# Kernel optimization log

Hardware: AMD Instinct MI355X
Metric: run time of the kernel (lower is better)

## Reference

```python
import jax, jax.numpy as jnp
import numpy as np

N, E, D, L = 50000, 640000, 128, 3  # nodes, edges, channels, layers
EPS = 1e-5


def setup_inputs() -> dict:
    key = jax.random.key(0)
    ks = jax.random.split(key, 10)
    s = 1.0 / np.sqrt(D)
    inp = {
        "x": jax.random.normal(ks[0], (N, D), dtype=jnp.float32),
        "edge_attr": jax.random.normal(ks[1], (E, D), dtype=jnp.float32),
        "w_self": jax.random.normal(ks[2], (L, D, D), dtype=jnp.float32) * s,
        "b_self": jnp.zeros((L, D), dtype=jnp.float32),
        "w_in": jax.random.normal(ks[3], (L, D, D), dtype=jnp.float32) * s,
        "b_in": jnp.zeros((L, D), dtype=jnp.float32),
        "w_rel": jax.random.normal(ks[4], (L, D, D), dtype=jnp.float32) * s,
        "b_rel": jnp.zeros((L, D), dtype=jnp.float32),
        "bn_gamma": jnp.ones((L - 1, D), dtype=jnp.float32),
        "bn_beta": jnp.zeros((L - 1, D), dtype=jnp.float32),
        "edge_index": jax.random.randint(ks[5], (2, E), 0, N, dtype=jnp.int64),
    }
    return inp


def _batchnorm(h, gamma, beta):
    mu = jnp.mean(h, axis=0)
    var = jnp.mean(jnp.square(h - mu), axis=0)  # biased var (torch BN training)
    return (h - mu) * jax.lax.rsqrt(var + EPS) * gamma + beta


def reference(x, edge_attr, w_self, b_self, w_in, b_in, w_rel, b_rel,
              bn_gamma, bn_beta, edge_index):
    src, dst = edge_index[0], edge_index[1]
    # per-node in-degree for mean aggregation (zero-degree nodes -> 0)
    cnt = jax.ops.segment_sum(jnp.ones((E, 1), x.dtype), dst, num_segments=N)
    denom = jnp.maximum(cnt, 1.0)
    for i in range(L):
        # message: lin_in(x_j * edge_attr)
        msg = jnp.einsum('ed,fd->ef', x[src] * edge_attr, w_in[i]) + b_in[i]
        agg = jax.ops.segment_sum(msg, dst, num_segments=N) / denom  # scatter-mean
        x = agg + jnp.einsum('nd,fd->nf', x, w_self[i]) + b_self[i]
        edge_attr = jnp.einsum('ed,fd->ef', edge_attr, w_rel[i]) + b_rel[i]
        if i < L - 1:
            x = jax.nn.relu(_batchnorm(x, bn_gamma[i], bn_beta[i]))
            # dropout p=0.0 -> identity
    return (x, edge_attr)
```

## Files before the change

### kernel.cpp

```cpp
#include <hip/hip_runtime.h>

#define DD 128

typedef __attribute__((ext_vector_type(8))) short bf16x8;
typedef __attribute__((ext_vector_type(4))) short bf16x4;
typedef __attribute__((ext_vector_type(4))) float f32x4;
typedef unsigned short u16;

__device__ __forceinline__ unsigned short f2bf(float f) {
  union { float f; unsigned u; } v; v.f = f;
  unsigned u = v.u;
  return (unsigned short)((u + 0x7FFFu + ((u >> 16) & 1u)) >> 16);
}
__device__ __forceinline__ float bf2f(unsigned short h) {
  union { unsigned u; float f; } v; v.u = ((unsigned)h) << 16; return v.f;
}
__device__ __forceinline__ bf16x8 pack8(f32x4 a, f32x4 b) {
  bf16x8 r;
  r[0] = (short)f2bf(a.x); r[1] = (short)f2bf(a.y);
  r[2] = (short)f2bf(a.z); r[3] = (short)f2bf(a.w);
  r[4] = (short)f2bf(b.x); r[5] = (short)f2bf(b.y);
  r[6] = (short)f2bf(b.z); r[7] = (short)f2bf(b.w);
  return r;
}

__device__ __forceinline__ bool idx_is64(const int* p) {
  return (p[1] | p[3] | p[5] | p[7]) == 0;
}
__device__ __forceinline__ int ld_idx(const int* p, long long i, bool is64) {
  return is64 ? (int)((const long long*)p)[i] : p[i];
}

__global__ void k_count(const int* __restrict__ idx, int* __restrict__ cnt, int E) {
  int e = blockIdx.x * blockDim.x + threadIdx.x;
  if (e >= E) return;
  bool is64 = idx_is64(idx);
  int d = ld_idx(idx, (long long)E + e, is64);
  atomicAdd(&cnt[d], 1);
}

__global__ __launch_bounds__(1024) void k_scan(const int* __restrict__ cnt,
    int* __restrict__ row_start, int* __restrict__ cursor, int N) {
  __shared__ int part[1024];
  int t = threadIdx.x;
  int chunk = (N + 1023) >> 10;
  int lo = t * chunk, hi = lo + chunk; if (hi > N) hi = N; if (lo > N) lo = N;
  int s = 0;
  for (int i = lo; i < hi; ++i) s += cnt[i];
  part[t] = s;
  __syncthreads();
  for (int off = 1; off < 1024; off <<= 1) {
    int v = (t >= off) ? part[t - off] : 0;
    __syncthreads();
    part[t] += v;
    __syncthreads();
  }
  int run = (t == 0) ? 0 : part[t - 1];
  for (int i = lo; i < hi; ++i) {
    row_start[i] = run; cursor[i] = run; run += cnt[i];
  }
  if (t == 1023) row_start[N] = part[1023];
}

__global__ void k_fill(const int* __restrict__ idx, int* __restrict__ cursor,
                       int* __restrict__ edge_of, int* __restrict__ src_csr, int E) {
  int e = blockIdx.x * blockDim.x + threadIdx.x;
  if (e >= E) return;
  bool is64 = idx_is64(idx);
  int s = ld_idx(idx, e, is64);
  int d = ld_idx(idx, (long long)E + e, is64);
  int pos = atomicAdd(&cursor[d], 1);
  edge_of[pos] = e;
  src_csr[pos] = s;
}

template <int MODE>
__global__ __launch_bounds__(256, 2) void k_relmsg(
    const float* __restrict__ x0, const u16* __restrict__ xbin,
    const float* __restrict__ ea0, const u16* __restrict__ eain,
    u16* __restrict__ eabout, float* __restrict__ eafout,
    u16* __restrict__ m,
    const int* __restrict__ edge_of, const int* __restrict__ src_csr,
    const float* __restrict__ w_rel, const float* __restrict__ b_rel,
    const float* __restrict__ scale, const float* __restrict__ shift,
    int ntE) {
  __shared__ short Wl[16384];
  for (int q = threadIdx.x; q < 4096; q += 256) {
    int off = q * 4;
    int f = off >> 7, d = off & 127;
    f32x4 w = *(const f32x4*)(w_rel + off);
    unsigned byte = ((unsigned)(f * 256 + d * 2)) ^ (unsigned)((f & 7) << 4);
    bf16x4 s4;
    s4[0] = (short)f2bf(w.x); s4[1] = (short)f2bf(w.y);
    s4[2] = (short)f2bf(w.z); s4[3] = (short)f2bf(w.w);
    *(bf16x4*)((char*)Wl + byte) = s4;
  }
  __syncthreads();
  int wave = threadIdx.x >> 6, lane = threadIdx.x & 63;
  int tile = blockIdx.x * 4 + wave;
  if (tile >= ntE) return;
  int r = lane & 15, g = lane >> 4;
  int k0 = tile * 16;
  int pos = r;
  int co = pos * 8;

  bf16x8 a8[4];
  if constexpr (MODE == 0) {
    int er = edge_of[k0 + r];
    const float* rp = ea0 + (size_t)er * DD;
#pragma unroll
    for (int ks = 0; ks < 4; ++ks) {
      const float* p = rp + ks * 32 + g * 8;
      a8[ks] = pack8(*(const f32x4*)p, *(const f32x4*)(p + 4));
    }
  } else {
    const u16* rp = eain + (size_t)(k0 + r) * DD;
#pragma unroll
    for (int ks = 0; ks < 4; ++ks) a8[ks] = *(const bf16x8*)(rp + ks * 32 + g * 8);
  }

  int kk[4], sn[4];
#pragma unroll
  for (int i = 0; i < 4; ++i) { kk[i] = k0 + g + 4 * i; sn[i] = src_csr[kk[i]]; }
  f32x4 xf0[4], xf1[4], ef0[4], ef1[4];
  bf16x8 xb[4], eb[4];
  if constexpr (MODE == 0) {
#pragma unroll
    for (int i = 0; i < 4; ++i) {
      int ei = edge_of[kk[i]];
      const float* xp = x0 + (size_t)sn[i] * DD + co;
      const float* ep = ea0 + (size_t)ei * DD + co;
      xf0[i] = *(const f32x4*)xp; xf1[i] = *(const f32x4*)(xp + 4);
      ef0[i] = *(const f32x4*)ep; ef1[i] = *(const f32x4*)(ep + 4);
    }
  } else {
#pragma unroll
    for (int i = 0; i < 4; ++i) {
      xb[i] = *(const bf16x8*)(xbin + (size_t)sn[i] * DD + co);
      eb[i] = *(const bf16x8*)(eain + (size_t)kk[i] * DD + co);
    }
  }
  float sc[8], sh[8];
  if constexpr (MODE >= 1) {
    f32x4 s0 = *(const f32x4*)(scale + co), s1 = *(const f32x4*)(scale + co + 4);
    f32x4 h0 = *(const f32x4*)(shift + co), h1 = *(const f32x4*)(shift + co + 4);
#pragma unroll
    for (int j = 0; j < 4; ++j) { sc[j] = s0[j]; sc[4 + j] = s1[j]; sh[j] = h0[j]; sh[4 + j] = h1[j]; }
  }

  f32x4 acc[8];
#pragma unroll
  for (int ct = 0; ct < 8; ++ct) acc[ct] = (f32x4){0.f, 0.f, 0.f, 0.f};
#pragma unroll
  for (int ct = 0; ct < 8; ++ct) {
    int f = ct * 16 + r;
    unsigned base = (unsigned)(f * 256);
    unsigned sw = (unsigned)((f & 7) << 4);
#pragma unroll
    for (int ks = 0; ks < 4; ++ks) {
      unsigned byte = (base + (unsigned)(ks * 64 + g * 16)) ^ sw;
      bf16x8 bb = *(const bf16x8*)((const char*)Wl + byte);
      acc[ct] = __builtin_amdgcn_mfma_f32_16x16x32_bf16(a8[ks], bb, acc[ct], 0, 0, 0);
    }
  }

#pragma unroll
  for (int i = 0; i < 4; ++i) {
    bf16x8 mm;
    if constexpr (MODE == 0) {
      f32x4 p0 = xf0[i] * ef0[i], p1 = xf1[i] * ef1[i];
      mm = pack8(p0, p1);
    } else {
#pragma unroll
      for (int j = 0; j < 8; ++j) {
        float xv = fmaxf(bf2f((u16)xb[i][j]) * sc[j] + sh[j], 0.f);
        mm[j] = (short)f2bf(xv * bf2f((u16)eb[i][j]));
      }
    }
    *(bf16x8*)(m + (size_t)kk[i] * DD + co) = mm;
  }

  size_t orow[4];
#pragma unroll
  for (int j = 0; j < 4; ++j) {
    int kr = k0 + g * 4 + j;
    orow[j] = (MODE == 2) ? (size_t)edge_of[kr] : (size_t)kr;
  }
#pragma unroll
  for (int ct = 0; ct < 8; ++ct) {
    int col = ct * 16 + r;
    float bv = b_rel[col];
#pragma unroll
    for (int j = 0; j < 4; ++j) {
      float v = acc[ct][j] + bv;
      if constexpr (MODE == 2) eafout[orow[j] * DD + col] = v;
      else                     eabout[orow[j] * DD + col] = f2bf(v);
    }
  }
}

__global__ __launch_bounds__(256) void k_segsum(const u16* __restrict__ m,
    const int* __restrict__ row_start, u16* __restrict__ agg, int N) {
  int n = blockIdx.x * 4 + (threadIdx.x >> 6);
  if (n >= N) return;
  int lane = threadIdx.x & 63;
  int e4 = lane >> 4, c = lane & 15, co = c * 8;
  int s0 = row_start[n], s1 = row_start[n + 1];
  int len = s1 - s0;
  float acc[8];
#pragma unroll
  for (int j = 0; j < 8; ++j) acc[j] = 0.f;
  for (int kk = e4; kk < len; kk += 4) {
    bf16x8 mv = *(const bf16x8*)(m + (size_t)(s0 + kk) * DD + co);
#pragma unroll
    for (int j = 0; j < 8; ++j) acc[j] += bf2f((u16)mv[j]);
  }
#pragma unroll
  for (int j = 0; j < 8; ++j) {
    float s = acc[j];
    s += __shfl_xor(s, 16);
    s += __shfl_xor(s, 32);
    acc[j] = s;
  }
  if (e4 == 0) {
    float inv = (len > 0) ? 1.0f / (float)len : 0.0f;
    f32x4 lo, hi;
#pragma unroll
    for (int j = 0; j < 4; ++j) { lo[j] = acc[j] * inv; hi[j] = acc[4 + j] * inv; }
    *(bf16x8*)(agg + (size_t)n * DD + co) = pack8(lo, hi);
  }
}

template <typename TX, bool BN, typename TO, bool STATS>
__global__ __launch_bounds__(256, 2) void k_node(const u16* __restrict__ agg,
    const TX* __restrict__ xc, const float* __restrict__ W_in,
    const float* __restrict__ W_self, const float* __restrict__ b_in,
    const float* __restrict__ b_self, const int* __restrict__ row_start,
    const float* __restrict__ scale, const float* __restrict__ shift,
    TO* __restrict__ xn, float* __restrict__ gsum, float* __restrict__ gssq,
    int ntiles) {
  __shared__ short Wl[DD * 256];
  for (int q = threadIdx.x; q < DD * 256 / 4; q += 256) {
    int off = q * 4;
    int f = off >> 8, k = off & 255;
    f32x4 w = (k < 128) ? *(const f32x4*)(W_in + f * 128 + k)
                        : *(const f32x4*)(W_self + f * 128 + (k - 128));
    unsigned byte = ((unsigned)(f * 512 + k * 2)) ^ (unsigned)((f & 7) << 4);
    bf16x4 s4;
    s4[0] = (short)f2bf(w.x); s4[1] = (short)f2bf(w.y);
    s4[2] = (short)f2bf(w.z); s4[3] = (short)f2bf(w.w);
    *(bf16x4*)((char*)Wl + byte) = s4;
  }
  __syncthreads();
  int wave = threadIdx.x >> 6, lane = threadIdx.x & 63;
  int tile = blockIdx.x * 4 + wave;
  if (tile >= ntiles) return;
  int r = lane & 15, g = lane >> 4;
  int arowi = tile * 16 + r;
  const u16* arow = agg + (size_t)arowi * DD;
  const TX* xrow = xc + (size_t)arowi * DD;
  bf16x8 a[8];
#pragma unroll
  for (int ks = 0; ks < 4; ++ks) a[ks] = *(const bf16x8*)(arow + ks * 32 + g * 8);
#pragma unroll
  for (int ks = 0; ks < 4; ++ks) {
    int c0 = ks * 32 + g * 8;
    if constexpr (sizeof(TX) == 2) {
      bf16x8 raw = *(const bf16x8*)(xrow + c0);
      if constexpr (BN) {
        bf16x8 fr;
#pragma unroll
        for (int j = 0; j < 8; ++j) {
          float f = fmaxf(bf2f((u16)raw[j]) * scale[c0 + j] + shift[c0 + j], 0.f);
          fr[j] = (short)f2bf(f);
        }
        a[4 + ks] = fr;
      } else {
        a[4 + ks] = raw;
      }
    } else {
      const float* p = (const float*)xrow + c0;
      a[4 + ks] = pack8(*(const f32x4*)p, *(const f32x4*)(p + 4));
    }
  }
  f32x4 acc[8];
#pragma unroll
  for (int ct = 0; ct < 8; ++ct) acc[ct] = (f32x4){0.f, 0.f, 0.f, 0.f};
#pragma unroll
  for (int ct = 0; ct < 8; ++ct) {
    int f = ct * 16 + r;
    unsigned base = (unsigned)(f * 512);
    unsigned sw = (unsigned)((f & 7) << 4);
#pragma unroll
    for (int ks = 0; ks < 8; ++ks) {
      unsigned byte = (base + (unsigned)(ks * 64 + g * 16)) ^ sw;
      bf16x8 b = *(const bf16x8*)((const char*)Wl + byte);
      acc[ct] = __builtin_amdgcn_mfma_f32_16x16x32_bf16(a[ks], b, acc[ct], 0, 0, 0);
    }
  }
  int nbase = tile * 16;
  float degmask[4];
#pragma unroll
  for (int j = 0; j < 4; ++j) {
    int nn = nbase + g * 4 + j;
    degmask[j] = (row_start[nn + 1] > row_start[nn]) ? 1.0f : 0.0f;
  }
#pragma unroll
  for (int ct = 0; ct < 8; ++ct) {
    int col = ct * 16 + r;
    float bi = b_in[col], bs = b_self[col];
    float s = 0.f, s2 = 0.f;
#pragma unroll
    for (int j = 0; j < 4; ++j) {
      float v = acc[ct][j] + bs + bi * degmask[j];
      if constexpr (sizeof(TO) == 2) xn[(size_t)(nbase + g * 4 + j) * DD + col] = (TO)f2bf(v);
      else                            xn[(size_t)(nbase + g * 4 + j) * DD + col] = (TO)v;
      s += v; s2 += v * v;
    }
    if constexpr (STATS) {
      s += __shfl_xor(s, 16);  s += __shfl_xor(s, 32);
      s2 += __shfl_xor(s2, 16); s2 += __shfl_xor(s2, 32);
      if (g == 0) { atomicAdd(&gsum[col], s); atomicAdd(&gssq[col], s2); }
    }
  }
}

__global__ void k_bnfin(float* __restrict__ gsum, float* __restrict__ gssq,
    const float* __restrict__ gamma, const float* __restrict__ beta,
    float* __restrict__ scale, float* __restrict__ shift, int N) {
  int d = threadIdx.x;
  float mu = gsum[d] / (float)N;
  float var = gssq[d] / (float)N - mu * mu;
  float rs = rsqrtf(var + 1e-5f);
  float sc = rs * gamma[d];
  scale[d] = sc;
  shift[d] = beta[d] - mu * sc;
  gsum[d] = 0.f;
  gssq[d] = 0.f;
}

static inline size_t alignup(size_t v, size_t a) { return (v + a - 1) & ~(a - 1); }

extern "C" void kernel_launch(void* const* d_in, const int* in_sizes, int n_in,
                              void* d_out, int out_size, void* d_ws, size_t ws_size,
                              hipStream_t stream) {
  const float* x0     = (const float*)d_in[0];
  const float* ea0    = (const float*)d_in[1];
  const float* w_self = (const float*)d_in[2];
  const float* b_self = (const float*)d_in[3];
  const float* w_in   = (const float*)d_in[4];
  const float* b_in   = (const float*)d_in[5];
  const float* w_rel  = (const float*)d_in[6];
  const float* b_rel  = (const float*)d_in[7];
  const float* gamma  = (const float*)d_in[8];
  const float* beta   = (const float*)d_in[9];
  const int*   idx    = (const int*)d_in[10];

  const int N = in_sizes[0] / DD;
  const int E = in_sizes[1] / DD;

  char* w = (char*)d_ws;
  size_t off = 0;
  int* cnt       = (int*)(w + off); off = alignup(off + (size_t)N * 4, 256);
  int* row_start = (int*)(w + off); off = alignup(off + (size_t)(N + 1) * 4, 256);
  int* cursor    = (int*)(w + off); off = alignup(off + (size_t)N * 4, 256);
  int* edge_of   = (int*)(w + off); off = alignup(off + (size_t)E * 4, 256);
  int* src_csr   = (int*)(w + off); off = alignup(off + (size_t)E * 4, 256);
  float* gstats  = (float*)(w + off); off = alignup(off + 256 * 4, 256);
  float* scale   = (float*)(w + off); off = alignup(off + 128 * 4, 256);
  float* shift   = (float*)(w + off); off = alignup(off + 128 * 4, 256);
  u16* agg       = (u16*)(w + off); off = alignup(off + (size_t)N * DD * 2, 256);
  u16* xbA       = (u16*)(w + off); off = alignup(off + (size_t)N * DD * 2, 256);
  u16* xbB       = (u16*)(w + off); off = alignup(off + (size_t)N * DD * 2, 256);
  u16* eaA       = (u16*)(w + off); off = alignup(off + (size_t)E * DD * 2, 256);
  u16* eaB       = (u16*)(w + off); off = alignup(off + (size_t)E * DD * 2, 256);
  u16* mbuf      = (u16*)(w + off); off = alignup(off + (size_t)E * DD * 2, 256);
  float* gsum = gstats, *gssq = gstats + 128;
  (void)ws_size; (void)n_in; (void)out_size;

  float* out_x  = (float*)d_out;
  float* out_ea = out_x + (size_t)N * DD;

  (void)hipMemsetAsync(cnt, 0, (size_t)N * 4, stream);
  int ethreads = 256, eblocks = (E + ethreads - 1) / ethreads;
  k_count<<<eblocks, ethreads, 0, stream>>>(idx, cnt, E);
  k_scan<<<1, 1024, 0, stream>>>(cnt, row_start, cursor, N);
  k_fill<<<eblocks, ethreads, 0, stream>>>(idx, cursor, edge_of, src_csr, E);
  (void)hipMemsetAsync(gstats, 0, 256 * 4, stream);

  const int ntN = N / 16;
  const int ntE = E / 16;
  const int rmBlocks = (ntE + 3) / 4;
  const int segBlocks = (N + 3) / 4;
  const int nodeBlocks = (ntN + 3) / 4;

  k_relmsg<0><<<rmBlocks, 256, 0, stream>>>(x0, nullptr, ea0, nullptr,
      eaA, nullptr, mbuf, edge_of, src_csr, w_rel, b_rel, scale, shift, ntE);
  k_segsum<<<segBlocks, 256, 0, stream>>>(mbuf, row_start, agg, N);
  k_node<float, false, u16, true><<<nodeBlocks, 256, 0, stream>>>(agg, x0,
      w_in, w_self, b_in, b_self, row_start, scale, shift, xbA, gsum, gssq, ntN);
  k_bnfin<<<1, 128, 0, stream>>>(gsum, gssq, gamma, beta, scale, shift, N);

  k_relmsg<1><<<rmBlocks, 256, 0, stream>>>(nullptr, xbA, nullptr, eaA,
      eaB, nullptr, mbuf, edge_of, src_csr,
      w_rel + DD * DD, b_rel + DD, scale, shift, ntE);
  k_segsum<<<segBlocks, 256, 0, stream>>>(mbuf, row_start, agg, N);
  k_node<u16, true, u16, true><<<nodeBlocks, 256, 0, stream>>>(agg, xbA,
      w_in + DD * DD, w_self + DD * DD, b_in + DD, b_self + DD,
      row_start, scale, shift, xbB, gsum, gssq, ntN);
  k_bnfin<<<1, 128, 0, stream>>>(gsum, gssq, gamma + DD, beta + DD, scale, shift, N);

  k_relmsg<2><<<rmBlocks, 256, 0, stream>>>(nullptr, xbB, nullptr, eaB,
      nullptr, out_ea, mbuf, edge_of, src_csr,
      w_rel + 2 * DD * DD, b_rel + 2 * DD, scale, shift, ntE);
  k_segsum<<<segBlocks, 256, 0, stream>>>(mbuf, row_start, agg, N);
  k_node<u16, true, float, false><<<nodeBlocks, 256, 0, stream>>>(agg, xbB,
      w_in + 2 * DD * DD, w_self + 2 * DD * DD, b_in + 2 * DD, b_self + 2 * DD,
      row_start, scale, shift, out_x, gsum, gssq, ntN);
}
```

Measured before the change: 1.136 ms.

## Process edges in source-sorted order and scatter messages to dst-CSR positions

Edges are now ordered by source node for the message/relation kernel, so x[src] gathers hit the same rows consecutively and gain cache locality. A permutation array maps each source-sorted edge to its destination-CSR slot, and messages are written there so segment-sum still reads contiguous rows. This adds a second count, scan and cursor pass in the preprocessing, one more index load per edge, and scattered writes of the message rows. The edge_attr working layout also changes from dst-sorted to src-sorted order across layers.

```diff
diff --git a/kernel.cpp b/kernel.cpp
--- a/kernel.cpp
+++ b/kernel.cpp
@@ -31,16 +31,19 @@
   return is64 ? (int)((const long long*)p)[i] : p[i];
 }
 
-__global__ void k_count(const int* __restrict__ idx, int* __restrict__ cnt, int E) {
+__global__ void k_count(const int* __restrict__ idx, int* __restrict__ cntD,
+                        int* __restrict__ cntS, int E) {
   int e = blockIdx.x * blockDim.x + threadIdx.x;
   if (e >= E) return;
   bool is64 = idx_is64(idx);
+  int s = ld_idx(idx, e, is64);
   int d = ld_idx(idx, (long long)E + e, is64);
-  atomicAdd(&cnt[d], 1);
+  atomicAdd(&cntD[d], 1);
+  atomicAdd(&cntS[s], 1);
 }
 
 __global__ __launch_bounds__(1024) void k_scan(const int* __restrict__ cnt,
-    int* __restrict__ row_start, int* __restrict__ cursor, int N) {
+    int* __restrict__ base, int* __restrict__ cursor, int N) {
   __shared__ int part[1024];
   int t = threadIdx.x;
   int chunk = (N + 1023) >> 10;
@@ -57,30 +60,34 @@
   }
   int run = (t == 0) ? 0 : part[t - 1];
   for (int i = lo; i < hi; ++i) {
-    row_start[i] = run; cursor[i] = run; run += cnt[i];
-  }
-  if (t == 1023) row_start[N] = part[1023];
-}
-
-__global__ void k_fill(const int* __restrict__ idx, int* __restrict__ cursor,
-                       int* __restrict__ edge_of, int* __restrict__ src_csr, int E) {
+    base[i] = run; cursor[i] = run; run += cnt[i];
+  }
+  if (t == 1023) base[N] = part[1023];
+}
+
+__global__ void k_fill(const int* __restrict__ idx, int* __restrict__ cursorD,
+                       int* __restrict__ cursorS, int* __restrict__ ss_edge,
+                       int* __restrict__ ss_src, int* __restrict__ pos_csr, int E) {
   int e = blockIdx.x * blockDim.x + threadIdx.x;
   if (e >= E) return;
   bool is64 = idx_is64(idx);
   int s = ld_idx(idx, e, is64);
   int d = ld_idx(idx, (long long)E + e, is64);
-  int pos = atomicAdd(&cursor[d], 1);
-  edge_of[pos] = e;
-  src_csr[pos] = s;
+  int pd = atomicAdd(&cursorD[d], 1);
+  int ps = atomicAdd(&cursorS[s], 1);
+  ss_edge[ps] = e;
+  ss_src[ps] = s;
+  pos_csr[ps] = pd;
 }
 
 template <int MODE>
-__global__ __launch_bounds__(256, 2) void k_relmsg(
+__global__ __launch_bounds__(256, 2) void k_gm(
     const float* __restrict__ x0, const u16* __restrict__ xbin,
     const float* __restrict__ ea0, const u16* __restrict__ eain,
     u16* __restrict__ eabout, float* __restrict__ eafout,
     u16* __restrict__ m,
-    const int* __restrict__ edge_of, const int* __restrict__ src_csr,
+    const int* __restrict__ ss_edge, const int* __restrict__ ss_src,
+    const int* __restrict__ pos_csr,
     const float* __restrict__ w_rel, const float* __restrict__ b_rel,
     const float* __restrict__ scale, const float* __restrict__ shift,
     int ntE) {
@@ -101,12 +108,11 @@
   if (tile >= ntE) return;
   int r = lane & 15, g = lane >> 4;
   int k0 = tile * 16;
-  int pos = r;
-  int co = pos * 8;
+  int co = r * 8;
 
   bf16x8 a8[4];
   if constexpr (MODE == 0) {
-    int er = edge_of[k0 + r];
+    int er = ss_edge[k0 + r];
     const float* rp = ea0 + (size_t)er * DD;
 #pragma unroll
     for (int ks = 0; ks < 4; ++ks) {
@@ -119,15 +125,19 @@
     for (int ks = 0; ks < 4; ++ks) a8[ks] = *(const bf16x8*)(rp + ks * 32 + g * 8);
   }
 
-  int kk[4], sn[4];
-#pragma unroll
-  for (int i = 0; i < 4; ++i) { kk[i] = k0 + g + 4 * i; sn[i] = src_csr[kk[i]]; }
+  int kk[4], sn[4], pc[4];
+#pragma unroll
+  for (int i = 0; i < 4; ++i) {
+    kk[i] = k0 + g + 4 * i;
+    sn[i] = ss_src[kk[i]];
+    pc[i] = pos_csr[kk[i]];
+  }
   f32x4 xf0[4], xf1[4], ef0[4], ef1[4];
   bf16x8 xb[4], eb[4];
   if constexpr (MODE == 0) {
 #pragma unroll
     for (int i = 0; i < 4; ++i) {
-      int ei = edge_of[kk[i]];
+      int ei = ss_edge[kk[i]];
       const float* xp = x0 + (size_t)sn[i] * DD + co;
       const float* ep = ea0 + (size_t)ei * DD + co;
       xf0[i] = *(const f32x4*)xp; xf1[i] = *(const f32x4*)(xp + 4);
@@ -177,14 +187,14 @@
         mm[j] = (short)f2bf(xv * bf2f((u16)eb[i][j]));
       }
     }
-    *(bf16x8*)(m + (size_t)kk[i] * DD + co) = mm;
+    *(bf16x8*)(m + (size_t)pc[i] * DD + co) = mm;
   }
 
   size_t orow[4];
 #pragma unroll
   for (int j = 0; j < 4; ++j) {
     int kr = k0 + g * 4 + j;
-    orow[j] = (MODE == 2) ? (size_t)edge_of[kr] : (size_t)kr;
+    orow[j] = (MODE == 2) ? (size_t)ss_edge[kr] : (size_t)kr;
   }
 #pragma unroll
   for (int ct = 0; ct < 8; ++ct) {
@@ -361,11 +371,15 @@
 
   char* w = (char*)d_ws;
   size_t off = 0;
-  int* cnt       = (int*)(w + off); off = alignup(off + (size_t)N * 4, 256);
+  int* cntD      = (int*)(w + off); off = alignup(off + (size_t)N * 4, 256);
+  int* cntS      = (int*)(w + off); off = alignup(off + (size_t)N * 4, 256);
   int* row_start = (int*)(w + off); off = alignup(off + (size_t)(N + 1) * 4, 256);
-  int* cursor    = (int*)(w + off); off = alignup(off + (size_t)N * 4, 256);
-  int* edge_of   = (int*)(w + off); off = alignup(off + (size_t)E * 4, 256);
-  int* src_csr   = (int*)(w + off); off = alignup(off + (size_t)E * 4, 256);
+  int* col_start = (int*)(w + off); off = alignup(off + (size_t)(N + 1) * 4, 256);
+  int* cursorD   = (int*)(w + off); off = alignup(off + (size_t)N * 4, 256);
+  int* cursorS   = (int*)(w + off); off = alignup(off + (size_t)N * 4, 256);
+  int* ss_edge   = (int*)(w + off); off = alignup(off + (size_t)E * 4, 256);
+  int* ss_src    = (int*)(w + off); off = alignup(off + (size_t)E * 4, 256);
+  int* pos_csr   = (int*)(w + off); off = alignup(off + (size_t)E * 4, 256);
   float* gstats  = (float*)(w + off); off = alignup(off + 256 * 4, 256);
   float* scale   = (float*)(w + off); off = alignup(off + 128 * 4, 256);
   float* shift   = (float*)(w + off); off = alignup(off + 128 * 4, 256);
@@ -381,28 +395,32 @@
   float* out_x  = (float*)d_out;
   float* out_ea = out_x + (size_t)N * DD;
 
-  (void)hipMemsetAsync(cnt, 0, (size_t)N * 4, stream);
+  (void)hipMemsetAsync(cntD, 0, (size_t)N * 4, stream);
+  (void)hipMemsetAsync(cntS, 0, (size_t)N * 4, stream);
   int ethreads = 256, eblocks = (E + ethreads - 1) / ethreads;
-  k_count<<<eblocks, ethreads, 0, stream>>>(idx, cnt, E);
-  k_scan<<<1, 1024, 0, stream>>>(cnt, row_start, cursor, N);
-  k_fill<<<eblocks, ethreads, 0, stream>>>(idx, cursor, edge_of, src_csr, E);
+  k_count<<<eblocks, ethreads, 0, stream>>>(idx, cntD, cntS, E);
+  k_scan<<<1, 1024, 0, stream>>>(cntD, row_start, cursorD, N);
+  k_scan<<<1, 1024, 0, stream>>>(cntS, col_start, cursorS, N);
+  k_fill<<<eblocks, ethreads, 0, stream>>>(idx, cursorD, cursorS,
+      ss_edge, ss_src, pos_csr, E);
   (void)hipMemsetAsync(gstats, 0, 256 * 4, stream);
 
   const int ntN = N / 16;
   const int ntE = E / 16;
-  const int rmBlocks = (ntE + 3) / 4;
+  const int gmBlocks = (ntE + 3) / 4;
   const int segBlocks = (N + 3) / 4;
   const int nodeBlocks = (ntN + 3) / 4;
 
-  k_relmsg<0><<<rmBlocks, 256, 0, stream>>>(x0, nullptr, ea0, nullptr,
-      eaA, nullptr, mbuf, edge_of, src_csr, w_rel, b_rel, scale, shift, ntE);
+  k_gm<0><<<gmBlocks, 256, 0, stream>>>(x0, nullptr, ea0, nullptr,
+      eaA, nullptr, mbuf, ss_edge, ss_src, pos_csr,
+      w_rel, b_rel, scale, shift, ntE);
   k_segsum<<<segBlocks, 256, 0, stream>>>(mbuf, row_start, agg, N);
   k_node<float, false, u16, true><<<nodeBlocks, 256, 0, stream>>>(agg, x0,
       w_in, w_self, b_in, b_self, row_start, scale, shift, xbA, gsum, gssq, ntN);
   k_bnfin<<<1, 128, 0, stream>>>(gsum, gssq, gamma, beta, scale, shift, N);
 
-  k_relmsg<1><<<rmBlocks, 256, 0, stream>>>(nullptr, xbA, nullptr, eaA,
-      eaB, nullptr, mbuf, edge_of, src_csr,
+  k_gm<1><<<gmBlocks, 256, 0, stream>>>(nullptr, xbA, nullptr, eaA,
+      eaB, nullptr, mbuf, ss_edge, ss_src, pos_csr,
       w_rel + DD * DD, b_rel + DD, scale, shift, ntE);
   k_segsum<<<segBlocks, 256, 0, stream>>>(mbuf, row_start, agg, N);
   k_node<u16, true, u16, true><<<nodeBlocks, 256, 0, stream>>>(agg, xbA,
@@ -410,8 +428,8 @@
       row_start, scale, shift, xbB, gsum, gssq, ntN);
   k_bnfin<<<1, 128, 0, stream>>>(gsum, gssq, gamma + DD, beta + DD, scale, shift, N);
 
-  k_relmsg<2><<<rmBlocks, 256, 0, stream>>>(nullptr, xbB, nullptr, eaB,
-      nullptr, out_ea, mbuf, edge_of, src_csr,
+  k_gm<2><<<gmBlocks, 256, 0, stream>>>(nullptr, xbB, nullptr, eaB,
+      nullptr, out_ea, mbuf, ss_edge, ss_src, pos_csr,
       w_rel + 2 * DD * DD, b_rel + 2 * DD, scale, shift, ntE);
   k_segsum<<<segBlocks, 256, 0, stream>>>(mbuf, row_start, agg, N);
   k_node<u16, true, float, false><<<nodeBlocks, 256, 0, stream>>>(agg, xbB,
```

Result: slower. 1.329 ms (+17.0%).
